# Kernel optimization log

Hardware: AMD Instinct MI355X
Metric: run time of the kernel (lower is better)

The kernel has to match this reference:

```python
import jax, jax.numpy as jnp
import numpy as np

B, S = 2, 2048          # packed prefill: 2 sequences of 2048 tokens
T = B * S
HID = 3584
H, KV, D = 16, 8, 256   # query heads, kv heads, head_dim (num_groups = 2)
SCALE = 256.0 ** -0.5   # query_pre_attn_scalar ** -0.5
SOFTCAP = 50.0
WINDOW = 1024           # sliding_window (window_size_left)
ROPE_THETA = 10000.0


def _rope_cos_sin():
    # TGI PositionRotaryEmbedding: per-token cos/sin of shape [T, D//2]
    inv_freq = 1.0 / (ROPE_THETA ** (np.arange(0, D, 2, dtype=np.float32) / D))
    pos = np.tile(np.arange(S, dtype=np.float32), B)  # positions restart per sequence
    freqs = pos[:, None] * inv_freq[None, :]          # [T, D/2]
    return jnp.asarray(np.cos(freqs)), jnp.asarray(np.sin(freqs))


def _apply_rope(x, cos, sin):
    # neox-style rotate-half; x: [T, h, D], cos/sin: [T, D/2]
    x1, x2 = x[..., : D // 2], x[..., D // 2 :]
    c, s = cos[:, None, :], sin[:, None, :]
    return jnp.concatenate([x1 * c - x2 * s, x2 * c + x1 * s], axis=-1)


def setup_inputs() -> dict:
    key = jax.random.key(0)
    k1, k2, k3 = jax.random.split(key, 3)
    cos, sin = _rope_cos_sin()
    return {
        "hidden_states": jax.random.normal(k1, (T, HID), dtype=jnp.float32),
        "cos": cos,
        "sin": sin,
        "w_qkv": jax.random.normal(k2, ((H + 2 * KV) * D, HID), dtype=jnp.float32) * 0.02,
        "w_o": jax.random.normal(k3, (HID, H * D), dtype=jnp.float32) * 0.02,
    }


def reference(hidden_states, cos, sin, w_qkv, w_o):
    qkv = hidden_states @ w_qkv.T                      # [T, (H+2KV)*D]
    q = qkv[:, : H * D].reshape(T, H, D)
    k = qkv[:, H * D : (H + KV) * D].reshape(T, KV, D)
    v = qkv[:, (H + KV) * D :].reshape(T, KV, D)

    q = _apply_rope(q, cos, sin)
    k = _apply_rope(k, cos, sin)

    # unpack varlen batch (equal-length sequences)
    q = q.reshape(B, S, H, D)
    # GQA: repeat each kv head num_groups=2 times (kv_head_mapping)
    k = jnp.repeat(k.reshape(B, S, KV, D), H // KV, axis=2)
    v = jnp.repeat(v.reshape(B, S, KV, D), H // KV, axis=2)

    scores = jnp.einsum("bqhd,bkhd->bhqk", q, k) * SCALE
    scores = SOFTCAP * jnp.tanh(scores / SOFTCAP)      # logit softcapping

    i = jnp.arange(S)[:, None]
    j = jnp.arange(S)[None, :]
    allowed = (j <= i) & (j >= i - WINDOW)             # causal + sliding window left
    scores = jnp.where(allowed[None, None], scores, jnp.finfo(scores.dtype).min)

    probs = jax.nn.softmax(scores, axis=-1)
    out = jnp.einsum("bhqk,bkhd->bqhd", probs, v)      # [B, S, H, D]
    return out.reshape(T, H * D) @ w_o.T               # [T, HID]
```

## Files before the change

kernel.cpp:

```cpp
#include <hip/hip_runtime.h>

typedef __bf16 bf16x8 __attribute__((ext_vector_type(8)));
typedef __bf16 bf16x4 __attribute__((ext_vector_type(4)));
typedef float  f32x4  __attribute__((ext_vector_type(4)));

#define AS1 __attribute__((address_space(1)))
#define AS3 __attribute__((address_space(3)))

__device__ __forceinline__ void async16(const void* g, void* l) {
  __builtin_amdgcn_global_load_lds((const AS1 void*)g, (AS3 void*)l, 16, 0, 0);
}

static constexpr int T_   = 4096;
static constexpr int Sq   = 2048;
static constexpr int HID  = 3584;
static constexpr int NH   = 16;
static constexpr int NKV  = 8;
static constexpr int DH   = 256;
static constexpr float SCALE_   = 0.0625f;
static constexpr float SOFTCAP_ = 50.0f;
static constexpr int WINDOW_    = 1024;

__global__ __launch_bounds__(256) void cast2_f32_bf16(const float4* __restrict__ a,
                                                      bf16x4* __restrict__ oa, int n4a,
                                                      const float4* __restrict__ b,
                                                      bf16x4* __restrict__ ob, int n4b) {
  int i = blockIdx.x * 256 + threadIdx.x;
  int stride = gridDim.x * 256;
  int ntot = n4a + n4b;
  for (; i < ntot; i += stride) {
    const float4 v = (i < n4a) ? a[i] : b[i - n4a];
    bf16x4 o;
    o[0] = (__bf16)v.x; o[1] = (__bf16)v.y; o[2] = (__bf16)v.z; o[3] = (__bf16)v.w;
    if (i < n4a) oa[i] = o; else ob[i - n4a] = o;
  }
}


#define VMW(N) do { asm volatile("s_waitcnt vmcnt(" #N ")" ::: "memory"); \
                    __builtin_amdgcn_sched_barrier(0); } while (0)

#define BAR() do { asm volatile("" ::: "memory"); \
                   __builtin_amdgcn_s_barrier();  \
                   asm volatile("" ::: "memory"); } while (0)

#define RD_A(dst, SEL, CK, I0)                                                 \
  _Pragma("unroll") for (int ii_ = 0; ii_ < 4; ++ii_)                          \
    dst[ii_] = *(const bf16x8*)&lA[SEL][aBase + (CK) + ((I0) + ii_) * 1024];

#define RD_B(KK, SEL, CK)                                                      \
  _Pragma("unroll") for (int j_ = 0; j_ < 4; ++j_)                             \
    bfr[j_][KK] = *(const bf16x8*)&lB[SEL][bBase + (CK) + j_ * 1024];

#define MFMA4(aSet, KK, I0)                                                    \
  __builtin_amdgcn_s_setprio(1);                                               \
  _Pragma("unroll") for (int ii_ = 0; ii_ < 4; ++ii_)                          \
    _Pragma("unroll") for (int j_ = 0; j_ < 4; ++j_)                           \
      acc[(I0) + ii_][j_] = __builtin_amdgcn_mfma_f32_16x16x32_bf16(           \
          aSet[ii_], bfr[j_][KK], acc[(I0) + ii_][j_], 0, 0, 0);               \
  __builtin_amdgcn_s_setprio(0);

template <bool OUT_BF16>
__global__ __launch_bounds__(512, 2) void gemm_bt8(const __bf16* __restrict__ A,
                                                   const __bf16* __restrict__ B,
                                                   __bf16* __restrict__ Cb,
                                                   float* __restrict__ Cf,
                                                   int M, int N, int K) {
  __shared__ __attribute__((aligned(16))) __bf16 lA[2][256 * 64];
  __shared__ __attribute__((aligned(16))) __bf16 lB[2][256 * 64];

  const int tid  = threadIdx.x;
  const int w    = tid >> 6;
  const int lane = tid & 63;
  const int wm   = w >> 2;
  const int wn   = w & 3;
  const int mrow = lane & 15;
  const int quad = lane >> 4;
  const int sw   = mrow & 7;

  const int gx = gridDim.x, gy = gridDim.y;
  const int orig = blockIdx.y * gx + blockIdx.x;
  int tileN, tileM;
  {
    int ccols, crows;
    if ((gx % 4) == 0 && (gy % 2) == 0)      { ccols = 4; crows = 2; }
    else if ((gx % 2) == 0 && (gy % 4) == 0) { ccols = 2; crows = 4; }
    else                                     { ccols = 1; crows = 1; }
    if (ccols * crows == 8) {
      const int cw = gx / ccols, ch = gy / crows;
      const int xcd = orig & 7, loc = orig >> 3;
      const int cx = xcd % ccols, cy = xcd / ccols;
      const int ln = loc % cw,    lm = loc / cw;
      tileN = (cx * cw + ln) * 256;
      tileM = (cy * ch + lm) * 256;
    } else {
      tileN = blockIdx.x * 256;
      tileM = blockIdx.y * 256;
    }
  }

  const int srow   = tid >> 3;
  const int schunk = (tid & 7) ^ (srow & 7);
  const int k64  = K << 6;
  const int k128 = K << 7;
  const __bf16* pa = A + (size_t)(tileM + srow) * K + schunk * 8;
  const __bf16* pb = B + (size_t)(tileN + srow) * K + schunk * 8;

  auto stage_half = [&](__bf16* lbase, int lrow, const __bf16* lanePtr, int koff) {
    async16(lanePtr + koff,       &lbase[(lrow + w * 8) * 64]);
    async16(lanePtr + koff + k64, &lbase[(lrow + 64 + w * 8) * 64]);
  };

  const int cK0 = (quad ^ sw) * 8;
  const int cK1 = cK0 ^ 32;
  const int aBase = (wm * 128 + mrow) * 64;
  const int bBase = (wn * 64 + mrow) * 64;

  f32x4 acc[8][4];
#pragma unroll
  for (int i = 0; i < 8; ++i)
#pragma unroll
    for (int j = 0; j < 4; ++j) acc[i][j] = (f32x4){0.f, 0.f, 0.f, 0.f};

  const int NT = K >> 6;
  const int NI = NT >> 1;

  stage_half(lB[0], 0,   pb, 0);
  stage_half(lB[0], 128, pb, k128);
  stage_half(lA[0], 0,   pa, 0);
  stage_half(lA[0], 128, pa, k128);
  stage_half(lB[1], 0,   pb, 64);
  stage_half(lB[1], 128, pb, 64 + k128);
  VMW(4);
  BAR();

  bf16x8 aX[4], aY[4], bfr[4][2];
  RD_A(aX, 0, cK0, 0); RD_B(0, 0, cK0);

  for (int it = 0; it < NI; ++it) {
    const int t    = 2 * it;
    const bool more = (it + 1 < NI);
    const int kA1 = (t + 1) << 6;
    const int k2  = (t + 2) << 6;
    const int k3  = (t + 3) << 6;

    RD_A(aY, 0, cK1, 0); RD_B(1, 0, cK1);
    stage_half(lA[1], 0, pa, kA1);
    MFMA4(aX, 0, 0);
    BAR();
    RD_A(aX, 0, cK0, 4);
    stage_half(lA[1], 128, pa, kA1 + k128);
    MFMA4(aY, 1, 0);
    BAR();
    RD_A(aY, 0, cK1, 4);
    if (more) stage_half(lB[0], 0, pb, k2);
    MFMA4(aX, 0, 4);
    if (more) VMW(2); else VMW(0);
    BAR();
    RD_A(aX, 1, cK0, 0); RD_B(0, 1, cK0);
    if (more) stage_half(lB[0], 128, pb, k2 + k128);
    MFMA4(aY, 1, 4);
    BAR();
    RD_A(aY, 1, cK1, 0); RD_B(1, 1, cK1);
    if (more) stage_half(lA[0], 0, pa, k2);
    MFMA4(aX, 0, 0);
    BAR();
    RD_A(aX, 1, cK0, 4);
    if (more) stage_half(lA[0], 128, pa, k2 + k128);
    MFMA4(aY, 1, 0);
    BAR();
    RD_A(aY, 1, cK1, 4);
    if (more) stage_half(lB[1], 0, pb, k3);
    MFMA4(aX, 0, 4);
    if (more) VMW(2); else VMW(0);
    BAR();
    RD_A(aX, 0, cK0, 0); RD_B(0, 0, cK0);
    if (more) stage_half(lB[1], 128, pb, k3 + k128);
    MFMA4(aY, 1, 4);
    BAR();
  }

#pragma unroll
  for (int i = 0; i < 8; ++i) {
    const int row0 = tileM + wm * 128 + i * 16 + quad * 4;
#pragma unroll
    for (int j = 0; j < 4; ++j) {
      const int col = tileN + wn * 64 + j * 16 + mrow;
#pragma unroll
      for (int r = 0; r < 4; ++r) {
        if constexpr (OUT_BF16)
          Cb[(size_t)(row0 + r) * N + col] = (__bf16)acc[i][j][r];
        else
          Cf[(size_t)(row0 + r) * N + col] = acc[i][j][r];
      }
    }
  }
}

__global__ __launch_bounds__(256) void aux_fused(const __bf16* __restrict__ qkv,
                                                 const float* __restrict__ cosb,
                                                 const float* __restrict__ sinb,
                                                 __bf16* __restrict__ qout,
                                                 __bf16* __restrict__ kout,
                                                 __bf16* __restrict__ vt,
                                                 const float4* __restrict__ wo,
                                                 bf16x4* __restrict__ wo_bf) {
  __shared__ __bf16 tile[64][72];
  const int blk = blockIdx.x;
  const int tid = threadIdx.x;

  if (blk < 4096) {
    const int t = blk;
    const int b = t >> 11, s = t & (Sq - 1);
    const int d = tid & 127;
    const int half = tid >> 7;
    const float c  = cosb[t * 128 + d];
    const float sn = sinb[t * 128 + d];
    const size_t base = (size_t)t * 8192;
#pragma unroll
    for (int it = 0; it < 12; ++it) {
      int seg = it * 2 + half;
      float x1 = (float)qkv[base + seg * 256 + d];
      float x2 = (float)qkv[base + seg * 256 + 128 + d];
      float o1 = x1 * c - x2 * sn;
      float o2 = x2 * c + x1 * sn;
      if (seg < 16) {
        size_t o = ((size_t)(b * NH + seg) * Sq + s) * DH + d;
        qout[o] = (__bf16)o1;
        qout[o + 128] = (__bf16)o2;
      } else {
        int kvh = seg - 16;
        size_t o = ((size_t)(b * NKV + kvh) * Sq + s) * DH + d;
        kout[o] = (__bf16)o1;
        kout[o + 128] = (__bf16)o2;
      }
    }
  } else if (blk < 6144) {
    const int flat = blk - 4096;
    const int bx  = flat & 127;
    const int bkv = flat >> 7;
    const int b = bkv >> 3, kv = bkv & 7;
    const int st0 = (bx >> 2) * 64;
    const int dt0 = (bx & 3) * 64;
#pragma unroll
    for (int it = 0; it < 2; ++it) {
      int g = it * 256 + tid;
      int r = g >> 3, cc = (g & 7) * 8;
      const __bf16* src = qkv + (size_t)(b * Sq + st0 + r) * 8192 + 6144 + kv * 256 + dt0 + cc;
      bf16x8 v = *(const bf16x8*)src;
#pragma unroll
      for (int j = 0; j < 8; ++j) tile[r][cc + j] = v[j];
    }
    __syncthreads();
#pragma unroll
    for (int it = 0; it < 2; ++it) {
      int g = it * 256 + tid;
      int r = g >> 3, cc = (g & 7) * 8;
      bf16x8 v;
#pragma unroll
      for (int j = 0; j < 8; ++j) v[j] = tile[cc + j][r];
      *(bf16x8*)(vt + ((size_t)bkv * DH + dt0 + r) * Sq + st0 + cc) = v;
    }
  } else {
    const int n4 = HID * 4096 / 4;
    int i = (blk - 6144) * 256 + tid;
    const int stride = 1024 * 256;
    for (; i < n4; i += stride) {
      float4 v = wo[i];
      bf16x4 o;
      o[0] = (__bf16)v.x; o[1] = (__bf16)v.y; o[2] = (__bf16)v.z; o[3] = (__bf16)v.w;
      wo_bf[i] = o;
    }
  }
}

template <int MODE>
__device__ __forceinline__ void softcap_tile(const f32x4 sc[4], float lrun[4],
                                             __bf16* Pl, int pbase, int mrow,
                                             int kt, int qi) {
#pragma unroll
  for (int j = 0; j < 4; ++j) {
    const int kj = kt + j * 16 + mrow;
#pragma unroll
    for (int r = 0; r < 4; ++r) {
      float z = sc[j][r] * (SCALE_ / SOFTCAP_);
      float z2 = z * z;
      float u = __builtin_fmaf(z2, 0.13333333f, -0.33333333f);
      float th = z * __builtin_fmaf(z2, u, 1.0f);
      float pe = __builtin_fmaf(th, 72.134752f, -72.134752f);
      if (MODE == 1) pe = (kj <= qi + r) ? pe : -1000.0f;
      if (MODE == 2) pe = (kj >= qi + r - WINDOW_) ? pe : -1000.0f;
      float p = __builtin_amdgcn_exp2f(pe);
      lrun[r] += p;
      Pl[pbase + r * 72 + j * 16 + mrow] = (__bf16)p;
    }
  }
}

__global__ __launch_bounds__(256, 2) void attn_kernel(const __bf16* __restrict__ q,
                                                      const __bf16* __restrict__ k,
                                                      const __bf16* __restrict__ vt,
                                                      __bf16* __restrict__ out) {
  __shared__ __bf16 Kl[64 * 256];
  __shared__ __bf16 Vl[256 * 64];
  __shared__ __bf16 Pl[4 * 1152];

  const int bid0 = blockIdx.x;
  const int gidx = (bid0 & 7) * 128 + (bid0 >> 3);
  const int grp  = gidx >> 5;
  const int qt   = 31 - (gidx & 31);
  const int h    = grp & 15;
  const int b    = grp >> 4;
  const int kvh  = h >> 1;
  const int q0   = qt * 64;
  const int tid = threadIdx.x, w = tid >> 6, lane = tid & 63;
  const int mrow = lane & 15, quad = lane >> 4;
  const int sw = mrow & 7;

  bf16x8 qf[8];
  const __bf16* qbase = q + ((size_t)(b * NH + h) * Sq + q0 + w * 16 + mrow) * DH;
#pragma unroll
  for (int kf = 0; kf < 8; ++kf) qf[kf] = *(const bf16x8*)(qbase + kf * 32 + quad * 8);

  f32x4 o[16];
#pragma unroll
  for (int n = 0; n < 16; ++n) o[n] = (f32x4){0.f, 0.f, 0.f, 0.f};
  float lrun[4] = {0.f, 0.f, 0.f, 0.f};

  int kt_lo = q0 - WINDOW_; if (kt_lo < 0) kt_lo = 0;
  const __bf16* kbase = k + (size_t)(b * NKV + kvh) * Sq * DH;
  const __bf16* vbase = vt + (size_t)(b * NKV + kvh) * DH * Sq;
  const int qi = q0 + w * 16 + quad * 4;
  const int pbase = w * 1152 + quad * 4 * 72;

  for (int kt = kt_lo; kt <= q0; kt += 64) {
#pragma unroll
    for (int it = 0; it < 8; ++it) {
      int g = it * 256 + tid;
      int rk = g >> 5, uk = g & 31;
      const __bf16* gk = kbase + (size_t)(kt + rk) * DH + (uk ^ (rk & 7)) * 8;
      async16(gk, &Kl[(it * 256 + w * 64) * 8]);
    }
#pragma unroll
    for (int it = 0; it < 8; ++it) {
      int g = it * 256 + tid;
      int rv = g >> 3, uv = g & 7;
      const __bf16* gv = vbase + (size_t)rv * Sq + kt + (uv ^ (rv & 7)) * 8;
      async16(gv, &Vl[(it * 256 + w * 64) * 8]);
    }
    __syncthreads();

    f32x4 sc[4];
#pragma unroll
    for (int j = 0; j < 4; ++j) sc[j] = (f32x4){0.f, 0.f, 0.f, 0.f};
#pragma unroll
    for (int kf = 0; kf < 8; ++kf)
#pragma unroll
      for (int j = 0; j < 4; ++j) {
        bf16x8 kfr = *(const bf16x8*)&Kl[(j * 16 + mrow) * 256 + ((kf * 4 + quad) ^ sw) * 8];
        sc[j] = __builtin_amdgcn_mfma_f32_16x16x32_bf16(qf[kf], kfr, sc[j], 0, 0, 0);
      }

    if (kt == q0)                 softcap_tile<1>(sc, lrun, Pl, pbase, mrow, kt, qi);
    else if (kt == q0 - WINDOW_)  softcap_tile<2>(sc, lrun, Pl, pbase, mrow, kt, qi);
    else                          softcap_tile<0>(sc, lrun, Pl, pbase, mrow, kt, qi);

    bf16x8 pf0 = *(const bf16x8*)&Pl[w * 1152 + mrow * 72 + 0 * 32 + quad * 8];
    bf16x8 pf1 = *(const bf16x8*)&Pl[w * 1152 + mrow * 72 + 1 * 32 + quad * 8];

#pragma unroll
    for (int kk = 0; kk < 2; ++kk) {
      bf16x8 pf = kk ? pf1 : pf0;
#pragma unroll
      for (int n = 0; n < 16; ++n) {
        bf16x8 vf = *(const bf16x8*)&Vl[(n * 16 + mrow) * 64 + ((kk * 4 + quad) ^ sw) * 8];
        o[n] = __builtin_amdgcn_mfma_f32_16x16x32_bf16(pf, vf, o[n], 0, 0, 0);
      }
    }
    __syncthreads();
  }

#pragma unroll
  for (int m = 1; m < 16; m <<= 1)
#pragma unroll
    for (int r = 0; r < 4; ++r) lrun[r] += __shfl_xor(lrun[r], m, 64);

  float inv[4];
#pragma unroll
  for (int r = 0; r < 4; ++r) inv[r] = 1.f / lrun[r];
  const size_t trow = (size_t)(b * Sq + q0 + w * 16 + quad * 4);
#pragma unroll
  for (int n = 0; n < 16; ++n)
#pragma unroll
    for (int r = 0; r < 4; ++r)
      out[(trow + r) * 4096 + h * DH + n * 16 + mrow] = (__bf16)(o[n][r] * inv[r]);
}

extern "C" void kernel_launch(void* const* d_in, const int* in_sizes, int n_in,
                              void* d_out, int out_size, void* d_ws, size_t ws_size,
                              hipStream_t stream) {
  (void)in_sizes; (void)n_in; (void)out_size; (void)ws_size;
  const float* hs   = (const float*)d_in[0];
  const float* cosb = (const float*)d_in[1];
  const float* sinb = (const float*)d_in[2];
  const float* wqkv = (const float*)d_in[3];
  const float* wo   = (const float*)d_in[4];
  float* out = (float*)d_out;
  char* ws = (char*)d_ws;

  __bf16* hs_bf   = (__bf16*)(ws + 0);
  __bf16* wo_bf   = (__bf16*)(ws + 0);
  __bf16* wqkv_bf = (__bf16*)(ws + 29360128);
  __bf16* attn_bf = (__bf16*)(ws + 29360128);
  __bf16* qkv_bf  = (__bf16*)(ws + 88080384);
  __bf16* q_bf    = (__bf16*)(ws + 155189248);
  __bf16* k_bf    = (__bf16*)(ws + 188743680);
  __bf16* vt_bf   = (__bf16*)(ws + 205520896);

  cast2_f32_bf16<<<2048, 256, 0, stream>>>((const float4*)hs, (bf16x4*)hs_bf, T_ * HID / 4,
                                           (const float4*)wqkv, (bf16x4*)wqkv_bf, 8192 * HID / 4);

  gemm_bt8<true><<<dim3(8192 / 256, T_ / 256), 512, 0, stream>>>(
      hs_bf, wqkv_bf, qkv_bf, nullptr, T_, 8192, HID);

  aux_fused<<<7168, 256, 0, stream>>>(qkv_bf, cosb, sinb, q_bf, k_bf, vt_bf,
                                      (const float4*)wo, (bf16x4*)wo_bf);

  attn_kernel<<<dim3(2 * NH * (Sq / 64)), 256, 0, stream>>>(q_bf, k_bf, vt_bf, attn_bf);

  gemm_bt8<false><<<dim3(HID / 256, T_ / 256), 512, 0, stream>>>(
      attn_bf, wo_bf, nullptr, out, T_, HID, 4096);
}
```

Before: 709.6 us.

## Swap MFMA operands for vector epilogue stores and deepen GEMM prefetch pipeline

Swaps the A/B operands in the MFMA so each lane's accumulator holds four consecutive columns of one row. The epilogue can then write 8-byte bf16x4 or 16-byte f32x4 vector stores instead of four scalar strided stores. The LDS staging schedule is shifted one half-tile earlier, with one more half-tile issued in the prologue and the vmcnt waits relaxed from 2 to 4, so global loads run further ahead of compute. A sched_barrier after each MFMA group also pins instruction ordering. This adds more in-flight loads and constrains the compiler's scheduling, which could affect overlap.

```diff
diff --git a/kernel.cpp b/kernel.cpp
--- a/kernel.cpp
+++ b/kernel.cpp
@@ -52,13 +52,14 @@
   _Pragma("unroll") for (int j_ = 0; j_ < 4; ++j_)                             \
     bfr[j_][KK] = *(const bf16x8*)&lB[SEL][bBase + (CK) + j_ * 1024];
 
-#define MFMA4(aSet, KK, I0)                                                    \
+#define MFMA16(aSet, KK, I0)                                                   \
   __builtin_amdgcn_s_setprio(1);                                               \
   _Pragma("unroll") for (int ii_ = 0; ii_ < 4; ++ii_)                          \
     _Pragma("unroll") for (int j_ = 0; j_ < 4; ++j_)                           \
       acc[(I0) + ii_][j_] = __builtin_amdgcn_mfma_f32_16x16x32_bf16(           \
-          aSet[ii_], bfr[j_][KK], acc[(I0) + ii_][j_], 0, 0, 0);               \
-  __builtin_amdgcn_s_setprio(0);
+          bfr[j_][KK], aSet[ii_], acc[(I0) + ii_][j_], 0, 0, 0);               \
+  __builtin_amdgcn_s_setprio(0);                                               \
+  __builtin_amdgcn_sched_barrier(0);
 
 template <bool OUT_BF16>
 __global__ __launch_bounds__(512, 2) void gemm_bt8(const __bf16* __restrict__ A,
@@ -131,7 +132,8 @@
   stage_half(lA[0], 128, pa, k128);
   stage_half(lB[1], 0,   pb, 64);
   stage_half(lB[1], 128, pb, 64 + k128);
-  VMW(4);
+  stage_half(lA[1], 0,   pa, 64);
+  VMW(6);
   BAR();
 
   bf16x8 aX[4], aY[4], bfr[4][2];
@@ -145,53 +147,54 @@
     const int k3  = (t + 3) << 6;
 
     RD_A(aY, 0, cK1, 0); RD_B(1, 0, cK1);
-    stage_half(lA[1], 0, pa, kA1);
-    MFMA4(aX, 0, 0);
+    stage_half(lA[1], 128, pa, kA1 + k128);
+    MFMA16(aX, 0, 0);
     BAR();
     RD_A(aX, 0, cK0, 4);
-    stage_half(lA[1], 128, pa, kA1 + k128);
-    MFMA4(aY, 1, 0);
+    if (more) stage_half(lB[0], 0, pb, k2);
+    MFMA16(aY, 1, 0);
     BAR();
     RD_A(aY, 0, cK1, 4);
-    if (more) stage_half(lB[0], 0, pb, k2);
-    MFMA4(aX, 0, 4);
-    if (more) VMW(2); else VMW(0);
+    if (more) stage_half(lB[0], 128, pb, k2 + k128);
+    MFMA16(aX, 0, 4);
+    if (more) VMW(4); else VMW(0);
     BAR();
     RD_A(aX, 1, cK0, 0); RD_B(0, 1, cK0);
-    if (more) stage_half(lB[0], 128, pb, k2 + k128);
-    MFMA4(aY, 1, 4);
+    if (more) stage_half(lA[0], 0, pa, k2);
+    MFMA16(aY, 1, 4);
     BAR();
     RD_A(aY, 1, cK1, 0); RD_B(1, 1, cK1);
-    if (more) stage_half(lA[0], 0, pa, k2);
-    MFMA4(aX, 0, 0);
+    if (more) stage_half(lA[0], 128, pa, k2 + k128);
+    MFMA16(aX, 0, 0);
     BAR();
     RD_A(aX, 1, cK0, 4);
-    if (more) stage_half(lA[0], 128, pa, k2 + k128);
-    MFMA4(aY, 1, 0);
+    if (more) stage_half(lB[1], 0, pb, k3);
+    MFMA16(aY, 1, 0);
     BAR();
     RD_A(aY, 1, cK1, 4);
-    if (more) stage_half(lB[1], 0, pb, k3);
-    MFMA4(aX, 0, 4);
-    if (more) VMW(2); else VMW(0);
+    if (more) stage_half(lB[1], 128, pb, k3 + k128);
+    MFMA16(aX, 0, 4);
+    if (more) VMW(4); else VMW(0);
     BAR();
     RD_A(aX, 0, cK0, 0); RD_B(0, 0, cK0);
-    if (more) stage_half(lB[1], 128, pb, k3 + k128);
-    MFMA4(aY, 1, 4);
+    if (more) stage_half(lA[1], 0, pa, k3);
+    MFMA16(aY, 1, 4);
     BAR();
   }
 
 #pragma unroll
   for (int i = 0; i < 8; ++i) {
-    const int row0 = tileM + wm * 128 + i * 16 + quad * 4;
+    const int row = tileM + wm * 128 + i * 16 + mrow;
 #pragma unroll
     for (int j = 0; j < 4; ++j) {
-      const int col = tileN + wn * 64 + j * 16 + mrow;
-#pragma unroll
-      for (int r = 0; r < 4; ++r) {
-        if constexpr (OUT_BF16)
-          Cb[(size_t)(row0 + r) * N + col] = (__bf16)acc[i][j][r];
-        else
-          Cf[(size_t)(row0 + r) * N + col] = acc[i][j][r];
+      const int col = tileN + wn * 64 + j * 16 + quad * 4;
+      if constexpr (OUT_BF16) {
+        bf16x4 o;
+        o[0] = (__bf16)acc[i][j][0]; o[1] = (__bf16)acc[i][j][1];
+        o[2] = (__bf16)acc[i][j][2]; o[3] = (__bf16)acc[i][j][3];
+        *(bf16x4*)&Cb[(size_t)row * N + col] = o;
+      } else {
+        *(f32x4*)&Cf[(size_t)row * N + col] = acc[i][j];
       }
     }
   }
```

Result: no change. 705.5 us (-0.6%).
